# Kernel optimization log

Hardware: AMD Instinct MI355X
Metric: run time of the kernel (lower is better)

## Reference

```python
import jax, jax.numpy as jnp
import numpy as np

N_NODES = 100000
N_EDGES = 640000
D_IN = 128
D_OUT = 128


def setup_inputs() -> dict:
    key = jax.random.key(0)
    k1, k2, k3, k4, k5, k6 = jax.random.split(key, 6)
    x = jax.random.normal(k1, (N_NODES, D_IN), dtype=jnp.float32)
    edge_weights = jax.random.uniform(k2, (N_EDGES, 1), dtype=jnp.float32)
    src = jax.random.randint(k3, (N_EDGES,), 0, N_NODES)
    dst = jax.random.randint(k4, (N_EDGES,), 0, N_NODES)
    # nn.Linear init scale ~ 1/sqrt(in_feats)
    W = jax.random.normal(k5, (D_OUT, D_IN), dtype=jnp.float32) / np.sqrt(D_IN)
    b = jax.random.normal(k6, (D_OUT,), dtype=jnp.float32) / np.sqrt(D_IN)
    return {"x": x, "edge_weights": edge_weights, "src": src, "dst": dst, "W": W, "b": b}


def reference(x, edge_weights, src, dst, W, b):
    # message: gather source node features, scale by per-edge weight  [E, D]
    m = x[src] * edge_weights
    # reduce: sum messages into destination nodes  [N, D]
    h = jax.ops.segment_sum(m, dst, num_segments=N_NODES)
    # dense linear  [N, D_OUT]
    return h @ W.T + b
```

## Files before the change

### kernel.cpp

```cpp
#include <hip/hip_runtime.h>
#include <hip/hip_bf16.h>

#define D 128
#define SCAN_CH 4096
#define NP1 256
#define BSH 9

typedef __bf16 bf16x8 __attribute__((ext_vector_type(8)));
typedef float  f32x4  __attribute__((ext_vector_type(4)));
typedef float  f32x2  __attribute__((ext_vector_type(2)));

__device__ __forceinline__ __bf16 f2bf(float f) { return (__bf16)f; }
__device__ __forceinline__ int pad8(int v) { return (v + 7) & ~7; }

__global__ __launch_bounds__(256) void prep_kernel(
    const float* __restrict__ W, __bf16* __restrict__ wb,
    int* __restrict__ cnt, int M)
{
    int t = blockIdx.x * 256 + threadIdx.x;
    for (int i = t; i < M; i += gridDim.x * 256) cnt[i] = 0;

    if (t < 2048) {
        int lane = t & 63;
        int frag = t >> 6;
        int kb = frag >> 3, fn = frag & 7;
        int n  = fn * 16 + (lane & 15);
        int k0 = kb * 32 + (lane >> 4) * 8;
        const float* src = &W[(size_t)n * D + k0];
        float4 v0 = *reinterpret_cast<const float4*>(src);
        float4 v1 = *reinterpret_cast<const float4*>(src + 4);
        bf16x8 o;
        o[0]=f2bf(v0.x); o[1]=f2bf(v0.y); o[2]=f2bf(v0.z); o[3]=f2bf(v0.w);
        o[4]=f2bf(v1.x); o[5]=f2bf(v1.y); o[6]=f2bf(v1.z); o[7]=f2bf(v1.w);
        *reinterpret_cast<bf16x8*>(&wb[((size_t)frag * 64 + lane) * 8]) = o;
    }
}

__global__ __launch_bounds__(256) void gemm_p1a_kernel(
    const float* __restrict__ x, const __bf16* __restrict__ wb,
    __bf16* __restrict__ y, int M,
    const int* __restrict__ dst, int* __restrict__ cnt,
    int* __restrict__ cnts, int E, int chunk, int NBK)
{
    __shared__ int h[256];
    const int tid = threadIdx.x;

    if (blockIdx.x < NP1) {
        h[tid] = 0;
        __syncthreads();
        int s = blockIdx.x * chunk;
        int e = s + chunk < E ? s + chunk : E;
        for (int i = s + tid; i < e; i += 256) {
            int d = dst[i];
            atomicAdd(&cnt[d], 1);
            atomicAdd(&h[d >> BSH], 1);
        }
        __syncthreads();
        if (tid < NBK) cnts[(size_t)tid * NP1 + blockIdx.x] = h[tid];
        return;
    }

    const int gb   = blockIdx.x - NP1;
    const int lane = tid & 63;
    const int wv   = tid >> 6;
    const int l15  = lane & 15;
    const int l4   = lane >> 4;
    const int row_base = gb * 128 + wv * 32;
    if (row_base >= M) return;

    f32x4 acc[2][8];
    #pragma unroll
    for (int mi = 0; mi < 2; ++mi)
        #pragma unroll
        for (int fn = 0; fn < 8; ++fn)
            #pragma unroll
            for (int c = 0; c < 4; ++c) acc[mi][fn][c] = 0.f;

    #pragma unroll
    for (int kb = 0; kb < 4; ++kb) {
        bf16x8 b[8];
        #pragma unroll
        for (int fn = 0; fn < 8; ++fn)
            b[fn] = *reinterpret_cast<const bf16x8*>(
                        &wb[((size_t)(kb * 8 + fn) * 64 + lane) * 8]);
        #pragma unroll
        for (int mi = 0; mi < 2; ++mi) {
            int row = row_base + mi * 16 + l15;
            int rc  = row < M ? row : M - 1;
            const f32x4* ap = reinterpret_cast<const f32x4*>(
                                   &x[(size_t)rc * D + kb * 32 + l4 * 8]);
            f32x4 v0 = __builtin_nontemporal_load(ap);
            f32x4 v1 = __builtin_nontemporal_load(ap + 1);
            bf16x8 a;
            a[0]=f2bf(v0[0]); a[1]=f2bf(v0[1]); a[2]=f2bf(v0[2]); a[3]=f2bf(v0[3]);
            a[4]=f2bf(v1[0]); a[5]=f2bf(v1[1]); a[6]=f2bf(v1[2]); a[7]=f2bf(v1[3]);
            #pragma unroll
            for (int fn = 0; fn < 8; ++fn)
                acc[mi][fn] = __builtin_amdgcn_mfma_f32_16x16x32_bf16(
                                  a, b[fn], acc[mi][fn], 0, 0, 0);
        }
    }

    #pragma unroll
    for (int mi = 0; mi < 2; ++mi)
        #pragma unroll
        for (int r = 0; r < 4; ++r) {
            int row = row_base + mi * 16 + l4 * 4 + r;
            if (row >= M) continue;
            #pragma unroll
            for (int fn = 0; fn < 8; ++fn)
                y[(size_t)row * D + fn * 16 + l15] = f2bf(acc[mi][fn][r]);
        }
}

__global__ __launch_bounds__(256) void scan2_part_kernel(
    const int* __restrict__ cnt, int N,
    const int* __restrict__ cnts, int NC,
    int* __restrict__ bsumA, int* __restrict__ bsumB, int NB_A)
{
    __shared__ int wred[4];
    const int tid  = threadIdx.x;
    const int lane = tid & 63;
    const int wid  = tid >> 6;
    const bool A   = (int)blockIdx.x < NB_A;
    const int blk  = A ? blockIdx.x : blockIdx.x - NB_A;
    int off = blk * SCAN_CH + tid * 16;
    int s = 0;
    #pragma unroll
    for (int i = 0; i < 16; ++i) {
        int idx = off + i;
        if (A) { if (idx < N)  s += pad8(cnt[idx]); }
        else   { if (idx < NC) s += cnts[idx]; }
    }
    #pragma unroll
    for (int d = 32; d >= 1; d >>= 1) s += __shfl_xor(s, d, 64);
    if (lane == 0) wred[wid] = s;
    __syncthreads();
    if (tid == 0) (A ? bsumA : bsumB)[blk] = wred[0] + wred[1] + wred[2] + wred[3];
}

__global__ __launch_bounds__(256) void scan2_write_kernel(
    const int* __restrict__ cnt, int N, int* __restrict__ base,
    const int* __restrict__ bsumA,
    const int* __restrict__ cnts, int NC, int* __restrict__ coffs,
    const int* __restrict__ bsumB, int NB_A)
{
    __shared__ int boff_s;
    __shared__ int wsum[4];
    const int tid  = threadIdx.x;
    const int lane = tid & 63;
    const int wid  = tid >> 6;
    const bool A   = (int)blockIdx.x < NB_A;
    const int blk  = A ? blockIdx.x : blockIdx.x - NB_A;

    if (wid == 0) {
        const int* bs = A ? bsumA : bsumB;
        int v = (lane < blk) ? bs[lane] : 0;
        #pragma unroll
        for (int d = 32; d >= 1; d >>= 1) v += __shfl_xor(v, d, 64);
        if (lane == 0) boff_s = v;
    }
    __syncthreads();

    int off = blk * SCAN_CH + tid * 16;
    int v[16];
    int s = 0;
    #pragma unroll
    for (int i = 0; i < 16; ++i) {
        int idx = off + i;
        if (A) v[i] = (idx < N)  ? pad8(cnt[idx]) : 0;
        else   v[i] = (idx < NC) ? cnts[idx] : 0;
        s += v[i];
    }
    int ssum = s;
    #pragma unroll
    for (int d = 1; d < 64; d <<= 1) {
        int t = __shfl_up(ssum, d, 64);
        if (lane >= d) ssum += t;
    }
    if (lane == 63) wsum[wid] = ssum;
    __syncthreads();
    int woff = 0;
    for (int w = 0; w < wid; ++w) woff += wsum[w];

    int run = boff_s + woff + ssum - s;
    #pragma unroll
    for (int i = 0; i < 16; ++i) {
        int idx = off + i;
        if (A) {
            if (idx < N) base[idx] = run;
            if (idx == N - 1) base[N] = run + v[i];
        } else {
            if (idx < NC) coffs[idx] = run;
        }
        run += v[i];
    }
}

__global__ __launch_bounds__(256) void p1b_kernel(
    const int* __restrict__ src, const int* __restrict__ dst,
    const float* __restrict__ ew, const int* __restrict__ coffs,
    int* __restrict__ cDst, int2* __restrict__ cSW, int E, int chunk, int NBK)
{
    __shared__ int h[256];
    const int tid = threadIdx.x;
    const int k   = blockIdx.x;
    if (tid < NBK) h[tid] = coffs[(size_t)tid * NP1 + k];
    __syncthreads();
    int s = k * chunk;
    int e = s + chunk < E ? s + chunk : E;
    for (int i = s + tid; i < e; i += 256) {
        int d  = dst[i];
        int p  = atomicAdd(&h[d >> BSH], 1);
        cDst[p] = d;
        cSW[p]  = make_int2(src[i] * (D / 2), __float_as_int(ew[i]));
    }
}

__global__ __launch_bounds__(256) void p2_kernel(
    const int* __restrict__ cDst, const int2* __restrict__ cSW,
    const int* __restrict__ coffs, const int* __restrict__ base,
    int2* __restrict__ bins, int M, int E, int NBK)
{
    __shared__ int cur[512];
    const int tid = threadIdx.x;
    const int b   = blockIdx.x;
    const int n0  = b << BSH;

    for (int ld = tid; ld < 512; ld += 256) {
        int n = n0 + ld;
        cur[ld] = (n < M) ? base[n] : 0;
    }
    __syncthreads();

    int e0 = coffs[(size_t)b * NP1];
    int e1 = (b + 1 < NBK) ? coffs[(size_t)(b + 1) * NP1] : E;
    for (int i = e0 + tid; i < e1; i += 256) {
        int ld = cDst[i] & 511;
        int p  = atomicAdd(&cur[ld], 1);
        bins[p] = cSW[i];
    }
    __syncthreads();

    const int2 z = make_int2(0, 0);
    for (int ld = tid; ld < 512; ld += 256) {
        int n = n0 + ld;
        if (n < M) {
            int end = base[n + 1];
            for (int p = cur[ld]; p < end; ++p) bins[p] = z;
        }
    }
}

__global__ __launch_bounds__(256) void gather_kernel(
    const __bf16* __restrict__ y, const int* __restrict__ base,
    const int2* __restrict__ bins, const float* __restrict__ bias,
    float* __restrict__ out, int N)
{
    int gw   = (blockIdx.x * 256 + threadIdx.x) >> 6;
    int lane = threadIdx.x & 63;
    if (gw >= N) return;

    const unsigned* yb = reinterpret_cast<const unsigned*>(y);
    const int b0 = __builtin_amdgcn_readfirstlane(base[gw]);
    const int b1 = __builtin_amdgcn_readfirstlane(base[gw + 1]);
    float accx = 0.f, accy = 0.f;

    for (int i = b0; i < b1; i += 8) {
        int2 e[8];
        #pragma unroll
        for (int t = 0; t < 8; ++t) e[t] = bins[i + t];
        unsigned p[8];
        #pragma unroll
        for (int t = 0; t < 8; ++t)
            p[t] = yb[(unsigned)e[t].x + lane];
        #pragma unroll
        for (int t = 0; t < 8; ++t) {
            float w = __int_as_float(e[t].y);
            accx += __uint_as_float(p[t] << 16) * w;
            accy += __uint_as_float(p[t] & 0xFFFF0000u) * w;
        }
    }

    float2 bv = *reinterpret_cast<const float2*>(&bias[lane * 2]);
    f32x2 o;
    o[0] = accx + bv.x;
    o[1] = accy + bv.y;
    __builtin_nontemporal_store(o, reinterpret_cast<f32x2*>(&out[(size_t)gw * D + lane * 2]));
}

extern "C" void kernel_launch(void* const* d_in, const int* in_sizes, int n_in,
                              void* d_out, int out_size, void* d_ws, size_t ws_size,
                              hipStream_t stream) {
    const float* x   = (const float*)d_in[0];
    const float* ew  = (const float*)d_in[1];
    const int*   src = (const int*)d_in[2];
    const int*   dst = (const int*)d_in[3];
    const float* W   = (const float*)d_in[4];
    const float* b   = (const float*)d_in[5];
    float*       out = (float*)d_out;

    const int E     = in_sizes[2];
    const int M     = out_size / D;
    const int NBK   = (M + 511) >> BSH;
    const int NC    = NBK * NP1;
    const int chunk = (E + NP1 - 1) / NP1;
    const int NB_A  = (M + SCAN_CH - 1) / SCAN_CH;
    const int NB_B  = (NC + SCAN_CH - 1) / SCAN_CH;
    const size_t BIN_CAP = (size_t)E + 7 * (size_t)M + 8;

    char* p = (char*)d_ws;
    __bf16* y     = (__bf16*)p;            p += (size_t)M * D * 2;
    __bf16* wb    = (__bf16*)p;            p += (size_t)32 * 64 * 8 * 2;
    int2*   bins  = (int2*)p;              p += BIN_CAP * 8;
    int*    base  = (int*)p;               p += (size_t)(M + 1) * 4;
    int*    cnt   = (int*)p;               p += (size_t)M * 4;
    int*    cnts  = (int*)p;               p += (size_t)NC * 4;
    int*    coffs = (int*)p;               p += (size_t)NC * 4;
    int*    cDst  = (int*)p;               p += (size_t)E * 4;
    int2*   cSW   = (int2*)p;              p += (size_t)E * 8;
    int*    bsumA = (int*)p;               p += 64 * 4;
    int*    bsumB = (int*)p;

    prep_kernel<<<64, 256, 0, stream>>>(W, wb, cnt, M);

    int gemmBlocks = (M + 127) / 128;
    gemm_p1a_kernel<<<NP1 + gemmBlocks, 256, 0, stream>>>(
        x, wb, y, M, dst, cnt, cnts, E, chunk, NBK);

    scan2_part_kernel<<<NB_A + NB_B, 256, 0, stream>>>(
        cnt, M, cnts, NC, bsumA, bsumB, NB_A);
    scan2_write_kernel<<<NB_A + NB_B, 256, 0, stream>>>(
        cnt, M, base, bsumA, cnts, NC, coffs, bsumB, NB_A);

    p1b_kernel<<<NP1, 256, 0, stream>>>(src, dst, ew, coffs, cDst, cSW, E, chunk, NBK);

    p2_kernel<<<NBK, 256, 0, stream>>>(cDst, cSW, coffs, base, bins, M, E, NBK);

    gather_kernel<<<(M * 64 + 255) / 256, 256, 0, stream>>>(y, base, bins, b, out, M);
}
```

Before: 122.3 us.

## Split histogram from GEMM and stage GEMM tiles through swizzled LDS

Splits the fused count-histogram and GEMM kernel into two separate launches. The GEMM now loads x rows with coalesced float4 reads into a swizzled shared-memory bf16 tile, feeds the MFMAs from LDS, and stages the output back through LDS so y is written as contiguous 16-byte stores instead of scattered 2-byte stores. The aim is better global memory coalescing for both x reads and y writes. The cost is an extra kernel launch, the loss of overlap between the atomic histogram pass and the GEMM, and 32 KB of LDS per block, which may limit occupancy.

```diff
diff --git a/kernel.cpp b/kernel.cpp
--- a/kernel.cpp
+++ b/kernel.cpp
@@ -7,6 +7,7 @@
 #define BSH 9
 
 typedef __bf16 bf16x8 __attribute__((ext_vector_type(8)));
+typedef __bf16 bf16x4 __attribute__((ext_vector_type(4)));
 typedef float  f32x4  __attribute__((ext_vector_type(4)));
 typedef float  f32x2  __attribute__((ext_vector_type(2)));
 
@@ -36,37 +37,51 @@
     }
 }
 
-__global__ __launch_bounds__(256) void gemm_p1a_kernel(
-    const float* __restrict__ x, const __bf16* __restrict__ wb,
-    __bf16* __restrict__ y, int M,
+__global__ __launch_bounds__(256) void p1a_kernel(
     const int* __restrict__ dst, int* __restrict__ cnt,
     int* __restrict__ cnts, int E, int chunk, int NBK)
 {
     __shared__ int h[256];
     const int tid = threadIdx.x;
-
-    if (blockIdx.x < NP1) {
-        h[tid] = 0;
-        __syncthreads();
-        int s = blockIdx.x * chunk;
-        int e = s + chunk < E ? s + chunk : E;
-        for (int i = s + tid; i < e; i += 256) {
-            int d = dst[i];
-            atomicAdd(&cnt[d], 1);
-            atomicAdd(&h[d >> BSH], 1);
-        }
-        __syncthreads();
-        if (tid < NBK) cnts[(size_t)tid * NP1 + blockIdx.x] = h[tid];
-        return;
-    }
-
-    const int gb   = blockIdx.x - NP1;
+    h[tid] = 0;
+    __syncthreads();
+    int s = blockIdx.x * chunk;
+    int e = s + chunk < E ? s + chunk : E;
+    for (int i = s + tid; i < e; i += 256) {
+        int d = dst[i];
+        atomicAdd(&cnt[d], 1);
+        atomicAdd(&h[d >> BSH], 1);
+    }
+    __syncthreads();
+    if (tid < NBK) cnts[(size_t)tid * NP1 + blockIdx.x] = h[tid];
+}
+
+__global__ __launch_bounds__(256) void gemm_kernel(
+    const float* __restrict__ x, const __bf16* __restrict__ wb,
+    __bf16* __restrict__ y, int M)
+{
+    __shared__ char xs[128 * 256];
+    const int tid  = threadIdx.x;
+    const int row0 = blockIdx.x * 128;
     const int lane = tid & 63;
     const int wv   = tid >> 6;
     const int l15  = lane & 15;
     const int l4   = lane >> 4;
-    const int row_base = gb * 128 + wv * 32;
-    if (row_base >= M) return;
+
+    #pragma unroll
+    for (int i = 0; i < 16; ++i) {
+        int f  = tid + i * 256;
+        int r  = f >> 5;
+        int c8 = f & 31;
+        int row = row0 + r;
+        int rc  = row < M ? row : M - 1;
+        f32x4 v = *reinterpret_cast<const f32x4*>(&x[(size_t)rc * D + c8 * 4]);
+        bf16x4 o;
+        o[0]=f2bf(v[0]); o[1]=f2bf(v[1]); o[2]=f2bf(v[2]); o[3]=f2bf(v[3]);
+        int byte = r * 256 + ((c8 * 8) ^ ((r & 7) << 4));
+        *reinterpret_cast<bf16x4*>(xs + byte) = o;
+    }
+    __syncthreads();
 
     f32x4 acc[2][8];
     #pragma unroll
@@ -85,32 +100,42 @@
                         &wb[((size_t)(kb * 8 + fn) * 64 + lane) * 8]);
         #pragma unroll
         for (int mi = 0; mi < 2; ++mi) {
-            int row = row_base + mi * 16 + l15;
-            int rc  = row < M ? row : M - 1;
-            const f32x4* ap = reinterpret_cast<const f32x4*>(
-                                   &x[(size_t)rc * D + kb * 32 + l4 * 8]);
-            f32x4 v0 = __builtin_nontemporal_load(ap);
-            f32x4 v1 = __builtin_nontemporal_load(ap + 1);
-            bf16x8 a;
-            a[0]=f2bf(v0[0]); a[1]=f2bf(v0[1]); a[2]=f2bf(v0[2]); a[3]=f2bf(v0[3]);
-            a[4]=f2bf(v1[0]); a[5]=f2bf(v1[1]); a[6]=f2bf(v1[2]); a[7]=f2bf(v1[3]);
+            int rl   = wv * 32 + mi * 16 + l15;
+            int byte = rl * 256 + ((kb * 64 + l4 * 16) ^ ((rl & 7) << 4));
+            bf16x8 a = *reinterpret_cast<const bf16x8*>(xs + byte);
             #pragma unroll
             for (int fn = 0; fn < 8; ++fn)
                 acc[mi][fn] = __builtin_amdgcn_mfma_f32_16x16x32_bf16(
                                   a, b[fn], acc[mi][fn], 0, 0, 0);
         }
     }
+    __syncthreads();
 
     #pragma unroll
     for (int mi = 0; mi < 2; ++mi)
         #pragma unroll
         for (int r = 0; r < 4; ++r) {
-            int row = row_base + mi * 16 + l4 * 4 + r;
-            if (row >= M) continue;
+            int rl = wv * 32 + mi * 16 + l4 * 4 + r;
             #pragma unroll
-            for (int fn = 0; fn < 8; ++fn)
-                y[(size_t)row * D + fn * 16 + l15] = f2bf(acc[mi][fn][r]);
-        }
+            for (int fn = 0; fn < 8; ++fn) {
+                int byte = rl * 256 + ((2 * (fn * 16 + l15)) ^ ((rl & 7) << 4));
+                *reinterpret_cast<__bf16*>(xs + byte) = f2bf(acc[mi][fn][r]);
+            }
+        }
+    __syncthreads();
+
+    #pragma unroll
+    for (int i = 0; i < 8; ++i) {
+        int g   = tid + i * 256;
+        int r   = g >> 4;
+        int c16 = g & 15;
+        int row = row0 + r;
+        if (row < M) {
+            int byte = r * 256 + ((c16 * 16) ^ ((r & 7) << 4));
+            bf16x8 v = *reinterpret_cast<const bf16x8*>(xs + byte);
+            *reinterpret_cast<bf16x8*>(&y[(size_t)row * D + c16 * 8]) = v;
+        }
+    }
 }
 
 __global__ __launch_bounds__(256) void scan2_part_kernel(
@@ -324,9 +349,9 @@
 
     prep_kernel<<<64, 256, 0, stream>>>(W, wb, cnt, M);
 
-    int gemmBlocks = (M + 127) / 128;
-    gemm_p1a_kernel<<<NP1 + gemmBlocks, 256, 0, stream>>>(
-        x, wb, y, M, dst, cnt, cnts, E, chunk, NBK);
+    p1a_kernel<<<NP1, 256, 0, stream>>>(dst, cnt, cnts, E, chunk, NBK);
+
+    gemm_kernel<<<(M + 127) / 128, 256, 0, stream>>>(x, wb, y, M);
 
     scan2_part_kernel<<<NB_A + NB_B, 256, 0, stream>>>(
         cnt, M, cnts, NC, bsumA, bsumB, NB_A);
```

Result: slower. 125.4 us (+2.6%).
